# Optimization experiments

Measured on AMD Instinct MI355X. Metric: run time of the kernel, lower is better.

The kernel has to match this reference:

```python
import jax, jax.numpy as jnp
import numpy as np

N = 50000      # nodes
E = 800000     # edges
G = 2000       # graphs
F_IN = 34
HID = 256
H = 8
D = 32         # HID // H
L = 5


def _layer_norm(x, g, b, eps=1e-5):
    m = x.mean(-1, keepdims=True)
    v = ((x - m) ** 2).mean(-1, keepdims=True)
    return (x - m) / jnp.sqrt(v + eps) * g + b


def _gelu(x):
    return jax.nn.gelu(x, approximate=False)  # torch exact GELU


def _segment_softmax(scores, seg, n):
    # scores: [E', H], seg: [E'] target node ids
    m = jax.ops.segment_max(scores, seg, num_segments=n)
    m = jnp.where(jnp.isfinite(m), m, 0.0)
    ex = jnp.exp(scores - m[seg])
    den = jax.ops.segment_sum(ex, seg, num_segments=n)
    return ex / (den[seg] + 1e-16)


def setup_inputs() -> dict:
    key = jax.random.key(0)
    ks = iter(jax.random.split(key, 64))

    def p(shape, fan):
        return (jax.random.normal(next(ks), shape, jnp.float32) / np.sqrt(fan)).astype(jnp.float32)

    inp = {}
    inp['x'] = jax.random.normal(next(ks), (N, F_IN), jnp.float32)
    inp['edge_index'] = jax.random.randint(next(ks), (2, E), 0, N, jnp.int32)
    inp['batch'] = jnp.sort(jax.random.randint(next(ks), (N,), 0, G, jnp.int32))

    # input embed
    inp['in_W'] = p((F_IN, HID), F_IN); inp['in_b'] = jnp.zeros((HID,), jnp.float32)
    inp['in_ln_g'] = jnp.ones((HID,), jnp.float32); inp['in_ln_b'] = jnp.zeros((HID,), jnp.float32)
    # 5 GATv2 layers (stacked on leading dim)
    inp['gat_Wl'] = p((L, HID, HID), HID); inp['gat_bl'] = jnp.zeros((L, HID), jnp.float32)
    inp['gat_Wr'] = p((L, HID, HID), HID); inp['gat_br'] = jnp.zeros((L, HID), jnp.float32)
    inp['gat_att'] = p((L, H, D), D)
    inp['gat_bias'] = jnp.zeros((L, HID), jnp.float32)
    inp['gat_ln_g'] = jnp.ones((L, HID), jnp.float32); inp['gat_ln_b'] = jnp.zeros((L, HID), jnp.float32)
    # TransformerConv
    inp['tr_Wq'] = p((HID, HID), HID); inp['tr_bq'] = jnp.zeros((HID,), jnp.float32)
    inp['tr_Wk'] = p((HID, HID), HID); inp['tr_bk'] = jnp.zeros((HID,), jnp.float32)
    inp['tr_Wv'] = p((HID, HID), HID); inp['tr_bv'] = jnp.zeros((HID,), jnp.float32)
    inp['tr_Wskip'] = p((HID, HID), HID); inp['tr_bskip'] = jnp.zeros((HID,), jnp.float32)
    inp['tr_ln_g'] = jnp.ones((HID,), jnp.float32); inp['tr_ln_b'] = jnp.zeros((HID,), jnp.float32)
    # output proj
    inp['out_W'] = p((2 * HID, 2 * HID), 2 * HID); inp['out_b'] = jnp.zeros((2 * HID,), jnp.float32)
    inp['out_ln_g'] = jnp.ones((2 * HID,), jnp.float32); inp['out_ln_b'] = jnp.zeros((2 * HID,), jnp.float32)
    return inp


def reference(x, edge_index, batch,
              in_W, in_b, in_ln_g, in_ln_b,
              gat_Wl, gat_bl, gat_Wr, gat_br, gat_att, gat_bias, gat_ln_g, gat_ln_b,
              tr_Wq, tr_bq, tr_Wk, tr_bk, tr_Wv, tr_bv, tr_Wskip, tr_bskip, tr_ln_g, tr_ln_b,
              out_W, out_b, out_ln_g, out_ln_b):
    # input embedding (dropout inactive in eval)
    h = _gelu(_layer_norm(x @ in_W + in_b, in_ln_g, in_ln_b))

    src, dst = edge_index[0], edge_index[1]  # PyG: row=source j, col=target i
    loops = jnp.arange(N, dtype=src.dtype)
    s2 = jnp.concatenate([src, loops])  # GATv2 adds self loops
    d2 = jnp.concatenate([dst, loops])

    for l in range(L):  # small fixed loop over layers
        xl = (h @ gat_Wl[l] + gat_bl[l]).reshape(N, H, D)  # source transform / message
        xr = (h @ gat_Wr[l] + gat_br[l]).reshape(N, H, D)  # target transform
        e = jax.nn.leaky_relu(xl[s2] + xr[d2], 0.2)        # [E', H, D]
        score = jnp.einsum('ehd,hd->eh', e, gat_att[l])
        alpha = _segment_softmax(score, d2, N)             # softmax over incoming edges
        out = jax.ops.segment_sum(xl[s2] * alpha[..., None], d2, num_segments=N)
        out = out.reshape(N, HID) + gat_bias[l]
        h = h + _gelu(_layer_norm(out, gat_ln_g[l], gat_ln_b[l]))

    # TransformerConv (no self loops, root_weight skip connection)
    q = (h @ tr_Wq + tr_bq).reshape(N, H, D)
    k = (h @ tr_Wk + tr_bk).reshape(N, H, D)
    v = (h @ tr_Wv + tr_bv).reshape(N, H, D)
    score = (q[dst] * k[src]).sum(-1) / jnp.sqrt(jnp.float32(D))  # [E, H]
    alpha = _segment_softmax(score, dst, N)
    out = jax.ops.segment_sum(v[src] * alpha[..., None], dst, num_segments=N).reshape(N, HID)
    out = out + h @ tr_Wskip + tr_bskip
    h = h + _layer_norm(out, tr_ln_g, tr_ln_b)

    # global mean + max pool
    cnt = jax.ops.segment_sum(jnp.ones((N,), h.dtype), batch, num_segments=G)
    h_mean = jax.ops.segment_sum(h, batch, num_segments=G) / jnp.maximum(cnt, 1.0)[:, None]
    h_max = jax.ops.segment_max(h, batch, num_segments=G)
    h_max = jnp.where(jnp.isfinite(h_max), h_max, 0.0)
    ge = jnp.concatenate([h_mean, h_max], axis=-1)  # [G, 512]
    return _gelu(_layer_norm(ge @ out_W + out_b, out_ln_g, out_ln_b))
```

## Files before the change

kernel.cpp:

```cpp
#include <hip/hip_runtime.h>
#include <math.h>

#define N_NODES 50000
#define N_EDGES 800000
#define N_GRAPH 2000
#define F_INPUT 34
#define HID 256
#define NLAYER 5

typedef __attribute__((ext_vector_type(8))) short short8;
typedef __attribute__((ext_vector_type(4))) float float4v;

__device__ __forceinline__ float gelu_f(float x) {
  return 0.5f * x * (1.0f + erff(x * 0.70710678118654752440f));
}
__device__ __forceinline__ unsigned short bfr(float f) {
  unsigned u = __float_as_uint(f);
  return (unsigned short)((u + 0x7fffu + ((u >> 16) & 1u)) >> 16);
}
__device__ __forceinline__ float b2f(unsigned short s) {
  return __uint_as_float(((unsigned)s) << 16);
}
__device__ __forceinline__ float b2f_lo(unsigned u) {
  return __uint_as_float(u << 16);
}
__device__ __forceinline__ float b2f_hi(unsigned u) {
  return __uint_as_float(u & 0xffff0000u);
}
__device__ __forceinline__ float4 ld4bf(const unsigned short* p) {
  ushort4 u = *(const ushort4*)p;
  float4 f;
  f.x = b2f(u.x); f.y = b2f(u.y); f.z = b2f(u.z); f.w = b2f(u.w);
  return f;
}
__device__ __forceinline__ void acp16(const unsigned short* g, unsigned short* l) {
  __builtin_amdgcn_global_load_lds(
      (const __attribute__((address_space(1))) void*)g,
      (__attribute__((address_space(3))) void*)l, 16, 0, 0);
}

__global__ __launch_bounds__(256) void embed_fused(
    const float* __restrict__ x, const float* __restrict__ W,
    const float* __restrict__ bias, const float* __restrict__ gam,
    const float* __restrict__ bet, float* __restrict__ h,
    unsigned short* __restrict__ hb) {
  __shared__ float xs[16][34];
  __shared__ float ys[16][264];
  int tid = threadIdx.x;
  int r0 = blockIdx.x * 16;
  float* xsf = &xs[0][0];
  for (int i = tid; i < 544; i += 256) xsf[i] = x[(size_t)r0 * 34 + i];
  __syncthreads();
  {
    int rr = tid >> 4;
    int c0 = (tid & 15) * 16;
    float acc[16];
#pragma unroll
    for (int j = 0; j < 16; j += 4) {
      float4 b4 = *(const float4*)&bias[c0 + j];
      acc[j] = b4.x; acc[j + 1] = b4.y; acc[j + 2] = b4.z; acc[j + 3] = b4.w;
    }
    for (int k = 0; k < 34; ++k) {
      float xv = xs[rr][k];
#pragma unroll
      for (int j = 0; j < 16; j += 4) {
        float4 w4 = *(const float4*)&W[(size_t)k * 256 + c0 + j];
        acc[j]     = fmaf(xv, w4.x, acc[j]);
        acc[j + 1] = fmaf(xv, w4.y, acc[j + 1]);
        acc[j + 2] = fmaf(xv, w4.z, acc[j + 2]);
        acc[j + 3] = fmaf(xv, w4.w, acc[j + 3]);
      }
    }
#pragma unroll
    for (int j = 0; j < 16; j += 4) {
      float4 o = {acc[j], acc[j + 1], acc[j + 2], acc[j + 3]};
      *(float4*)&ys[rr][c0 + j] = o;
    }
  }
  __syncthreads();
  int wv = tid >> 6, lane = tid & 63;
  for (int rr = wv * 4; rr < wv * 4 + 4; ++rr) {
    float4 v = *(const float4*)&ys[rr][lane * 4];
    float s = v.x + v.y + v.z + v.w;
    for (int o = 1; o < 64; o <<= 1) s += __shfl_xor(s, o);
    float mean = s * (1.f / 256.f);
    float d0 = v.x - mean, d1 = v.y - mean, d2 = v.z - mean, d3 = v.w - mean;
    float vs = d0 * d0 + d1 * d1 + d2 * d2 + d3 * d3;
    for (int o = 1; o < 64; o <<= 1) vs += __shfl_xor(vs, o);
    float inv = rsqrtf(vs * (1.f / 256.f) + 1e-5f);
    float4 g4 = *(const float4*)&gam[lane * 4];
    float4 b4 = *(const float4*)&bet[lane * 4];
    float y0 = gelu_f(d0 * inv * g4.x + b4.x);
    float y1 = gelu_f(d1 * inv * g4.y + b4.y);
    float y2 = gelu_f(d2 * inv * g4.z + b4.z);
    float y3 = gelu_f(d3 * inv * g4.w + b4.w);
    size_t idx = (size_t)(r0 + rr) * HID + lane * 4;
    float4 o4 = {y0, y1, y2, y3};
    *(float4*)&h[idx] = o4;
    ushort4 ob = {bfr(y0), bfr(y1), bfr(y2), bfr(y3)};
    *(ushort4*)&hb[idx] = ob;
  }
}

__global__ __launch_bounds__(256) void gemm_mfma(
    const unsigned short* __restrict__ A, const unsigned short* __restrict__ Bt,
    const float* __restrict__ bias, void* __restrict__ Cv,
    int M, int Nn, int K, int flags) {
  __shared__ unsigned short smem[16384];
  unsigned short* As = smem;
  unsigned short* Bs = smem + 8192;
  int tid = threadIdx.x;
  int wave = tid >> 6, lane = tid & 63;

  int gx = gridDim.x;
  int flat = blockIdx.y * gx + blockIdx.x;
  int nwg = gx * gridDim.y;
  int xcd = flat & 7, idx = flat >> 3;
  int qb = nwg >> 3, r = nwg & 7;
  int g0 = xcd * qb + min(xcd, r);
  int wk = g0 + idx;
  int row0 = (wk / gx) * 128;
  int col0 = (wk % gx) * 128;

  int wm0 = (wave >> 1) * 64;
  int wn0 = (wave & 1) * 64;
  int q = lane >> 4;
  int ln = lane & 15;

  int srow = wave * 8 + (lane >> 3);
  int scol = ((lane & 7) ^ (lane >> 3)) * 8;
  const unsigned short* pa[4];
  const unsigned short* pb[4];
  unsigned short* la[4];
  unsigned short* lb[4];
#pragma unroll
  for (int i = 0; i < 4; ++i) {
    int ra = min(row0 + srow + i * 32, M - 1);
    pa[i] = A + (size_t)ra * K + scol;
    pb[i] = Bt + (size_t)(col0 + srow + i * 32) * K + scol;
    la[i] = As + (i * 32 + wave * 8) * 64;
    lb[i] = Bs + (i * 32 + wave * 8) * 64;
  }

  float4v acc[4][4];
#pragma unroll
  for (int i = 0; i < 4; ++i)
#pragma unroll
    for (int j = 0; j < 4; ++j) acc[i][j] = (float4v)0.f;

  for (int k0 = 0; k0 < K; k0 += 64) {
#pragma unroll
    for (int i = 0; i < 4; ++i) acp16(pa[i] + k0, la[i]);
#pragma unroll
    for (int i = 0; i < 4; ++i) acp16(pb[i] + k0, lb[i]);
    __syncthreads();
#pragma unroll
    for (int ks = 0; ks < 2; ++ks) {
      int ch = ((ks * 4 + q) ^ (ln & 7)) * 8;
      short8 af[4], bf[4];
#pragma unroll
      for (int i = 0; i < 4; ++i)
        af[i] = *(const short8*)&As[(wm0 + i * 16 + ln) * 64 + ch];
#pragma unroll
      for (int j = 0; j < 4; ++j)
        bf[j] = *(const short8*)&Bs[(wn0 + j * 16 + ln) * 64 + ch];
#pragma unroll
      for (int i = 0; i < 4; ++i)
#pragma unroll
        for (int j = 0; j < 4; ++j)
          acc[i][j] = __builtin_amdgcn_mfma_f32_16x16x32_bf16(af[i], bf[j], acc[i][j], 0, 0, 0);
    }
    __syncthreads();
  }
  int rb = (lane >> 4) * 4;
  if (flags & 2) {
    unsigned short* Cb = (unsigned short*)Cv;
    unsigned short* eb = smem + wave * 2560;
#pragma unroll
    for (int p = 0; p < 2; ++p) {
#pragma unroll
      for (int jj = 0; jj < 2; ++jj) {
        int j = p * 2 + jj;
        float bv = bias[col0 + wn0 + j * 16 + ln];
#pragma unroll
        for (int i = 0; i < 4; ++i)
#pragma unroll
          for (int r2 = 0; r2 < 4; ++r2)
            eb[(i * 16 + rb + r2) * 40 + jj * 16 + ln] = bfr(acc[i][j][r2] + bv);
      }
      int grow = row0 + wm0 + lane;
      uint4 w0 = *(uint4*)&eb[lane * 40 + 0];
      uint4 w1 = *(uint4*)&eb[lane * 40 + 8];
      uint4 w2 = *(uint4*)&eb[lane * 40 + 16];
      uint4 w3 = *(uint4*)&eb[lane * 40 + 24];
      if (grow < M) {
        unsigned short* dst = Cb + (size_t)grow * Nn + col0 + wn0 + p * 32;
        *(uint4*)&dst[0] = w0;
        *(uint4*)&dst[8] = w1;
        *(uint4*)&dst[16] = w2;
        *(uint4*)&dst[24] = w3;
      }
    }
  } else {
    float* C = (float*)Cv;
#pragma unroll
    for (int j = 0; j < 4; ++j) {
      int col = col0 + wn0 + j * 16 + ln;
      float bv = bias[col];
#pragma unroll
      for (int i = 0; i < 4; ++i)
#pragma unroll
        for (int r2 = 0; r2 < 4; ++r2) {
          int row = row0 + wm0 + i * 16 + rb + r2;
          if (row < M) C[(size_t)row * Nn + col] = acc[i][j][r2] + bv;
        }
    }
  }
}

__global__ __launch_bounds__(256) void prep_all(
    const float* __restrict__ Wl, const float* __restrict__ Wr,
    const float* __restrict__ Wq, const float* __restrict__ Wk,
    const float* __restrict__ Wv, const float* __restrict__ Wsk,
    unsigned short* __restrict__ outw,
    const float* __restrict__ Wout, unsigned short* __restrict__ outwout,
    const float* __restrict__ bl, const float* __restrict__ br,
    const float* __restrict__ bq, const float* __restrict__ bk,
    const float* __restrict__ bv, const float* __restrict__ bsk,
    float* __restrict__ bcat) {
  __shared__ float t[32][33];
  int z = blockIdx.z;
  int rr0 = threadIdx.x >> 5, c = threadIdx.x & 31;
  if (z < 14) {
    if (blockIdx.x >= 8 || blockIdx.y >= 8) return;
    const float* W = (z < 10) ? (((z & 1) ? Wr : Wl) + (size_t)(z >> 1) * 65536)
                   : (z == 10) ? Wq : (z == 11) ? Wk : (z == 12) ? Wv : Wsk;
    int k0 = blockIdx.y * 32, n0 = blockIdx.x * 32;
    for (int rr = rr0; rr < 32; rr += 8)
      t[rr][c] = W[(size_t)(k0 + rr) * HID + n0 + c];
    __syncthreads();
    for (int rr = rr0; rr < 32; rr += 8) {
      int n = n0 + rr;
      size_t row;
      if (z == 11)      row = 11 * 256 + (size_t)((n >> 2) * 8 + (n & 3));
      else if (z == 12) row = 11 * 256 + (size_t)((n >> 2) * 8 + 4 + (n & 3));
      else              row = (size_t)z * 256 + n;
      outw[row * HID + k0 + c] = bfr(t[c][rr]);
    }
  } else if (z == 14) {
    int k0 = blockIdx.y * 32, n0 = blockIdx.x * 32;
    for (int rr = rr0; rr < 32; rr += 8)
      t[rr][c] = Wout[(size_t)(k0 + rr) * 512 + n0 + c];
    __syncthreads();
    for (int rr = rr0; rr < 32; rr += 8)
      outwout[(size_t)(n0 + rr) * 512 + k0 + c] = bfr(t[c][rr]);
  } else {
    if (blockIdx.y != 0 || blockIdx.x >= 14) return;
    int i = blockIdx.x * 256 + threadIdx.x;
    if (i < 2560) {
      int l = i >> 9, cc = i & 511;
      bcat[i] = (cc < 256) ? bl[l * 256 + cc] : br[l * 256 + (cc - 256)];
    } else if (i < 3584) {
      int j = i - 2560;
      float v;
      if (j < 256) {
        v = bq[j];
      } else if (j < 768) {
        int p = j - 256;
        int hi = p >> 3, lo = p & 7;
        v = (lo < 4) ? bk[hi * 4 + lo] : bv[hi * 4 + (lo - 4)];
      } else {
        v = bsk[j - 768];
      }
      bcat[i] = v;
    }
  }
}

__global__ __launch_bounds__(256) void ln_act(
    const float* __restrict__ in, const float* __restrict__ gam,
    const float* __restrict__ bet, float* __restrict__ out,
    unsigned short* __restrict__ outb,
    int n_rows, int width, int do_gelu) {
  int wid = blockIdx.x * 4 + (threadIdx.x >> 6);
  int lane = threadIdx.x & 63;
  if (wid >= n_rows) return;
  int chunks = width >> 8;
  float4 v[2];
  float s = 0.f;
  for (int c = 0; c < chunks; ++c) {
    int off = c * 256 + lane * 4;
    float4 t = *(const float4*)&in[(size_t)wid * width + off];
    v[c] = t;
    s += t.x + t.y + t.z + t.w;
  }
  for (int o = 1; o < 64; o <<= 1) s += __shfl_xor(s, o);
  float mean = s / (float)width;
  float vs = 0.f;
  for (int c = 0; c < chunks; ++c) {
    float dx = v[c].x - mean, dy = v[c].y - mean, dz = v[c].z - mean, dw = v[c].w - mean;
    vs += dx * dx + dy * dy + dz * dz + dw * dw;
  }
  for (int o = 1; o < 64; o <<= 1) vs += __shfl_xor(vs, o);
  float inv = rsqrtf(vs / (float)width + 1e-5f);
  for (int c = 0; c < chunks; ++c) {
    int off = c * 256 + lane * 4;
    float4 g4 = *(const float4*)&gam[off];
    float4 b4 = *(const float4*)&bet[off];
    float y[4] = {(v[c].x - mean) * inv * g4.x + b4.x,
                  (v[c].y - mean) * inv * g4.y + b4.y,
                  (v[c].z - mean) * inv * g4.z + b4.z,
                  (v[c].w - mean) * inv * g4.w + b4.w};
    if (do_gelu) {
#pragma unroll
      for (int i = 0; i < 4; ++i) y[i] = gelu_f(y[i]);
    }
    size_t idx = (size_t)wid * width + off;
    float4 o4 = {y[0], y[1], y[2], y[3]};
    *(float4*)&out[idx] = o4;
    if (outb) {
      ushort4 ob = {bfr(y[0]), bfr(y[1]), bfr(y[2]), bfr(y[3])};
      *(ushort4*)&outb[idx] = ob;
    }
  }
}

__global__ __launch_bounds__(256) void edge_count(const int* __restrict__ ei,
                                                  int* __restrict__ counts) {
  int e = blockIdx.x * 256 + threadIdx.x;
  if (e < N_EDGES) atomicAdd(&counts[ei[N_EDGES + e]], 1);
}

__global__ __launch_bounds__(1024) void scan1(const int* __restrict__ counts,
                                              int* __restrict__ indptr,
                                              int* __restrict__ bsums, int n) {
  __shared__ int sm[1024];
  int tid = threadIdx.x;
  int i = blockIdx.x * 1024 + tid;
  int v = (i < n) ? counts[i] : 0;
  sm[tid] = v;
  __syncthreads();
  for (int off = 1; off < 1024; off <<= 1) {
    int t = (tid >= off) ? sm[tid - off] : 0;
    __syncthreads();
    sm[tid] += t;
    __syncthreads();
  }
  if (i < n) indptr[i] = sm[tid] - v;
  if (tid == 1023) bsums[blockIdx.x] = sm[1023];
}

__global__ __launch_bounds__(256) void scan3(const int* __restrict__ bsums,
                                             int* __restrict__ indptr,
                                             int* __restrict__ cursor, int n) {
  __shared__ int pre;
  int i = blockIdx.x * 256 + threadIdx.x;
  if (threadIdx.x == 0) {
    int nb = blockIdx.x >> 2;
    int a = 0;
    for (int j = 0; j < nb; ++j) a += bsums[j];
    pre = a;
  }
  __syncthreads();
  if (i < n) {
    int v = indptr[i] + pre;
    indptr[i] = v;
    cursor[i] = v;
  }
  if (i == 0) indptr[n] = N_EDGES;
}

__global__ __launch_bounds__(256) void edge_scatter(const int* __restrict__ ei,
                                                    int* __restrict__ cursor,
                                                    int* __restrict__ esrc) {
  int e = blockIdx.x * 256 + threadIdx.x;
  if (e < N_EDGES) {
    int d = ei[N_EDGES + e];
    int p = atomicAdd(&cursor[d], 1);
    esrc[p] = ei[e];
  }
}

#define GAT_EDGE(f)                                                        \
  {                                                                        \
    float ex = f.x + xri.x; ex = fmaxf(ex, 0.2f * ex);                     \
    float ey = f.y + xri.y; ey = fmaxf(ey, 0.2f * ey);                     \
    float ez = f.z + xri.z; ez = fmaxf(ez, 0.2f * ez);                     \
    float ew = f.w + xri.w; ew = fmaxf(ew, 0.2f * ew);                     \
    float p = ex * a4.x + ey * a4.y + ez * a4.z + ew * a4.w;               \
    p += __shfl_xor(p, 1); p += __shfl_xor(p, 2); p += __shfl_xor(p, 4);   \
    float wgt = __expf(fminf(p - m0, 60.f));                               \
    ax = fmaf(wgt, f.x, ax); ay = fmaf(wgt, f.y, ay);                      \
    az = fmaf(wgt, f.z, az); aw = fmaf(wgt, f.w, aw);                      \
    lsum += wgt;                                                           \
  }

__global__ __launch_bounds__(256) void gat_agg(
    const unsigned short* __restrict__ xlr, const float* __restrict__ att,
    const int* __restrict__ indptr, const int* __restrict__ esrc,
    const float* __restrict__ pre_bias, const float* __restrict__ gam,
    const float* __restrict__ bet, float* __restrict__ h,
    unsigned short* __restrict__ hb) {
  int wid = blockIdx.x * 4 + (threadIdx.x >> 6);
  int lane = threadIdx.x & 63;
  if (wid >= N_NODES) return;
  float4 xri = ld4bf(&xlr[(size_t)wid * 512 + 256 + lane * 4]);
  float4 a4 = *(const float4*)&att[lane * 4];
  int beg = indptr[wid], end = indptr[wid + 1];

  float m0, lsum, ax, ay, az, aw;
  {
    float4 f = ld4bf(&xlr[(size_t)wid * 512 + lane * 4]);
    float ex = f.x + xri.x; ex = fmaxf(ex, 0.2f * ex);
    float ey = f.y + xri.y; ey = fmaxf(ey, 0.2f * ey);
    float ez = f.z + xri.z; ez = fmaxf(ez, 0.2f * ez);
    float ew = f.w + xri.w; ew = fmaxf(ew, 0.2f * ew);
    float p = ex * a4.x + ey * a4.y + ez * a4.z + ew * a4.w;
    p += __shfl_xor(p, 1); p += __shfl_xor(p, 2); p += __shfl_xor(p, 4);
    m0 = p; lsum = 1.f;
    ax = f.x; ay = f.y; az = f.z; aw = f.w;
  }
  const unsigned short* xbase = xlr + lane * 4;
  int e = beg;
  for (; e + 3 < end; e += 4) {
    int j0 = esrc[e], j1 = esrc[e + 1], j2 = esrc[e + 2], j3 = esrc[e + 3];
    float4 f0 = ld4bf(xbase + (size_t)j0 * 512);
    float4 f1 = ld4bf(xbase + (size_t)j1 * 512);
    float4 f2 = ld4bf(xbase + (size_t)j2 * 512);
    float4 f3 = ld4bf(xbase + (size_t)j3 * 512);
    GAT_EDGE(f0); GAT_EDGE(f1); GAT_EDGE(f2); GAT_EDGE(f3);
  }
  for (; e < end; ++e) {
    int j = esrc[e];
    float4 f = ld4bf(xbase + (size_t)j * 512);
    GAT_EDGE(f);
  }
  float inv = 1.f / (lsum + 1e-16f);
  float4 pb = *(const float4*)&pre_bias[lane * 4];
  float y0 = ax * inv + pb.x, y1 = ay * inv + pb.y;
  float y2 = az * inv + pb.z, y3 = aw * inv + pb.w;
  float s = y0 + y1 + y2 + y3;
  for (int o = 1; o < 64; o <<= 1) s += __shfl_xor(s, o);
  float mean = s * (1.f / 256.f);
  float d0 = y0 - mean, d1 = y1 - mean, d2 = y2 - mean, d3 = y3 - mean;
  float vs = d0 * d0 + d1 * d1 + d2 * d2 + d3 * d3;
  for (int o = 1; o < 64; o <<= 1) vs += __shfl_xor(vs, o);
  float inv2 = rsqrtf(vs * (1.f / 256.f) + 1e-5f);
  float4 g4 = *(const float4*)&gam[lane * 4];
  float4 b4 = *(const float4*)&bet[lane * 4];
  y0 = gelu_f(d0 * inv2 * g4.x + b4.x);
  y1 = gelu_f(d1 * inv2 * g4.y + b4.y);
  y2 = gelu_f(d2 * inv2 * g4.z + b4.z);
  y3 = gelu_f(d3 * inv2 * g4.w + b4.w);
  size_t idx = (size_t)wid * HID + lane * 4;
  float4 r4 = *(const float4*)&h[idx];
  y0 += r4.x; y1 += r4.y; y2 += r4.z; y3 += r4.w;
  float4 o4 = {y0, y1, y2, y3};
  *(float4*)&h[idx] = o4;
  ushort4 ob = {bfr(y0), bfr(y1), bfr(y2), bfr(y3)};
  *(ushort4*)&hb[idx] = ob;
}

#define TR_EDGE(u_)                                                         \
  {                                                                         \
    float p = qi.x * b2f_lo(u_.x);                                          \
    p = fmaf(qi.y, b2f_hi(u_.x), p);                                        \
    p = fmaf(qi.z, b2f_lo(u_.y), p);                                        \
    p = fmaf(qi.w, b2f_hi(u_.y), p);                                        \
    p += __shfl_xor(p, 1); p += __shfl_xor(p, 2); p += __shfl_xor(p, 4);    \
    float wgt = __expf(fminf(p, 60.f));                                     \
    ax = fmaf(wgt, b2f_lo(u_.z), ax); ay = fmaf(wgt, b2f_hi(u_.z), ay);     \
    az = fmaf(wgt, b2f_lo(u_.w), az); aw = fmaf(wgt, b2f_hi(u_.w), aw);     \
    lsum += wgt;                                                            \
  }

__global__ __launch_bounds__(256) void tr_agg(
    const unsigned short* __restrict__ qkv, const int* __restrict__ indptr,
    const int* __restrict__ esrc,
    const float* __restrict__ gam, const float* __restrict__ bet,
    float* __restrict__ h) {
  int wid = blockIdx.x * 4 + (threadIdx.x >> 6);
  int lane = threadIdx.x & 63;
  if (wid >= N_NODES) return;
  const float scale = 0.17677669529663687f;
  float4 qi = ld4bf(&qkv[(size_t)wid * 1024 + lane * 4]);
  qi.x *= scale; qi.y *= scale; qi.z *= scale; qi.w *= scale;
  const unsigned short* kvbase = qkv + 256 + lane * 8;
  int beg = indptr[wid], end = indptr[wid + 1];
  float lsum = 0.f;
  float ax = 0.f, ay = 0.f, az = 0.f, aw = 0.f;
  int e = beg;
  for (; e + 3 < end; e += 4) {
    int j0 = esrc[e], j1 = esrc[e + 1], j2 = esrc[e + 2], j3 = esrc[e + 3];
    uint4 u0 = *(const uint4*)(kvbase + (size_t)j0 * 1024);
    uint4 u1 = *(const uint4*)(kvbase + (size_t)j1 * 1024);
    uint4 u2 = *(const uint4*)(kvbase + (size_t)j2 * 1024);
    uint4 u3 = *(const uint4*)(kvbase + (size_t)j3 * 1024);
    TR_EDGE(u0); TR_EDGE(u1); TR_EDGE(u2); TR_EDGE(u3);
  }
  for (; e < end; ++e) {
    uint4 u0 = *(const uint4*)(kvbase + (size_t)esrc[e] * 1024);
    TR_EDGE(u0);
  }
  float inv = 1.f / (lsum + 1e-16f);
  size_t idx = (size_t)wid * HID + lane * 4;
  float4 sk = ld4bf(&qkv[(size_t)wid * 1024 + 768 + lane * 4]);
  float y0 = ax * inv + sk.x, y1 = ay * inv + sk.y;
  float y2 = az * inv + sk.z, y3 = aw * inv + sk.w;
  float s = y0 + y1 + y2 + y3;
  for (int o = 1; o < 64; o <<= 1) s += __shfl_xor(s, o);
  float mean = s * (1.f / 256.f);
  float d0 = y0 - mean, d1 = y1 - mean, d2 = y2 - mean, d3 = y3 - mean;
  float vs = d0 * d0 + d1 * d1 + d2 * d2 + d3 * d3;
  for (int o = 1; o < 64; o <<= 1) vs += __shfl_xor(vs, o);
  float inv2 = rsqrtf(vs * (1.f / 256.f) + 1e-5f);
  float4 g4 = *(const float4*)&gam[lane * 4];
  float4 b4 = *(const float4*)&bet[lane * 4];
  float4 r4 = *(const float4*)&h[idx];
  float4 o4;
  o4.x = r4.x + d0 * inv2 * g4.x + b4.x;
  o4.y = r4.y + d1 * inv2 * g4.y + b4.y;
  o4.z = r4.z + d2 * inv2 * g4.z + b4.z;
  o4.w = r4.w + d3 * inv2 * g4.w + b4.w;
  *(float4*)&h[idx] = o4;
}

__global__ __launch_bounds__(256) void graph_bounds(const int* __restrict__ batch,
                                                    int* __restrict__ gptr) {
  int i = blockIdx.x * 256 + threadIdx.x;
  if (i >= N_NODES) return;
  int b0 = batch[i];
  if (i == 0)
    for (int g = 0; g <= b0; ++g) gptr[g] = 0;
  int b1 = (i + 1 < N_NODES) ? batch[i + 1] : N_GRAPH;
  for (int g = b0 + 1; g <= b1; ++g) gptr[g] = i + 1;
}

__global__ __launch_bounds__(256) void pool_seg(
    const float* __restrict__ h, const int* __restrict__ gptr,
    unsigned short* __restrict__ geb) {
  int g = blockIdx.x, c = threadIdx.x;
  int s = gptr[g], e = gptr[g + 1];
  float sum = 0.f, mx = -INFINITY;
  for (int r = s; r < e; ++r) {
    float vv = h[(size_t)r * HID + c];
    sum += vv;
    mx = fmaxf(mx, vv);
  }
  int cnt = e - s;
  geb[(size_t)g * 512 + c] = bfr(sum / (float)max(cnt, 1));
  geb[(size_t)g * 512 + 256 + c] = bfr(cnt ? mx : 0.f);
}

static inline void mfma_launch(const unsigned short* A, const unsigned short* Bt,
                               const float* bias, void* C, int M, int Nn, int K,
                               int flags, hipStream_t s) {
  dim3 grid(Nn / 128, (M + 127) / 128);
  gemm_mfma<<<grid, 256, 0, s>>>(A, Bt, bias, C, M, Nn, K, flags);
}

extern "C" void kernel_launch(void* const* d_in, const int* in_sizes, int n_in,
                              void* d_out, int out_size, void* d_ws, size_t ws_size,
                              hipStream_t stream) {
  const float* x       = (const float*)d_in[0];
  const int*   ei      = (const int*)d_in[1];
  const int*   batch   = (const int*)d_in[2];
  const float* in_W    = (const float*)d_in[3];
  const float* in_b    = (const float*)d_in[4];
  const float* in_ln_g = (const float*)d_in[5];
  const float* in_ln_b = (const float*)d_in[6];
  const float* gat_Wl  = (const float*)d_in[7];
  const float* gat_bl  = (const float*)d_in[8];
  const float* gat_Wr  = (const float*)d_in[9];
  const float* gat_br  = (const float*)d_in[10];
  const float* gat_att = (const float*)d_in[11];
  const float* gat_bias= (const float*)d_in[12];
  const float* gat_ln_g= (const float*)d_in[13];
  const float* gat_ln_b= (const float*)d_in[14];
  const float* tr_Wq   = (const float*)d_in[15];
  const float* tr_bq   = (const float*)d_in[16];
  const float* tr_Wk   = (const float*)d_in[17];
  const float* tr_bk   = (const float*)d_in[18];
  const float* tr_Wv   = (const float*)d_in[19];
  const float* tr_bv   = (const float*)d_in[20];
  const float* tr_Wsk  = (const float*)d_in[21];
  const float* tr_bsk  = (const float*)d_in[22];
  const float* tr_ln_g = (const float*)d_in[23];
  const float* tr_ln_b = (const float*)d_in[24];
  const float* out_W   = (const float*)d_in[25];
  const float* out_b   = (const float*)d_in[26];
  const float* out_ln_g= (const float*)d_in[27];
  const float* out_ln_b= (const float*)d_in[28];

  char* w = (char*)d_ws;
  auto take = [&](size_t bytes) -> char* {
    char* p = w;
    w += (bytes + 255) & ~(size_t)255;
    return p;
  };
  const size_t NB = (size_t)N_NODES * HID * sizeof(float);
  float* h    = (float*)take(NB);
  unsigned short* hb  = (unsigned short*)take((size_t)N_NODES * HID * 2);
  unsigned short* xq  = (unsigned short*)take((size_t)N_NODES * 1024 * 2);
  unsigned short* wbuf= (unsigned short*)take((size_t)(14 * 65536 + 262144) * 2);
  float* bcat = (float*)take(3584 * sizeof(float));
  int* indptr = (int*)take((N_NODES + 1) * sizeof(int));
  int* cursor = (int*)take(N_NODES * sizeof(int));
  int* counts = (int*)take(N_NODES * sizeof(int));
  int* esrc   = (int*)take(N_EDGES * sizeof(int));
  int* bsums  = (int*)take(64 * sizeof(int));
  char* w2 = (char*)xq;
  auto take2 = [&](size_t bytes) -> char* {
    char* p = w2;
    w2 += (bytes + 255) & ~(size_t)255;
    return p;
  };
  int* gptr = (int*)take2((N_GRAPH + 1) * sizeof(int));
  unsigned short* geb = (unsigned short*)take2((size_t)N_GRAPH * 512 * 2);
  float* tbuf = (float*)take2((size_t)N_GRAPH * 512 * sizeof(float));

  const int EB = (N_EDGES + 255) / 256;
  const int WB = (N_NODES + 3) / 4;
  const int NSB = (N_NODES + 1023) / 1024;

  {
    dim3 g(16, 16, 16);
    prep_all<<<g, 256, 0, stream>>>(gat_Wl, gat_Wr, tr_Wq, tr_Wk, tr_Wv, tr_Wsk,
                                    wbuf, out_W, wbuf + (size_t)14 * 65536,
                                    gat_bl, gat_br, tr_bq, tr_bk, tr_bv, tr_bsk,
                                    bcat);
  }

  hipMemsetAsync(counts, 0, N_NODES * sizeof(int), stream);
  edge_count<<<EB, 256, 0, stream>>>(ei, counts);
  scan1<<<NSB, 1024, 0, stream>>>(counts, indptr, bsums, N_NODES);
  scan3<<<(N_NODES + 255) / 256, 256, 0, stream>>>(bsums, indptr, cursor, N_NODES);
  edge_scatter<<<EB, 256, 0, stream>>>(ei, cursor, esrc);

  embed_fused<<<N_NODES / 16, 256, 0, stream>>>(x, in_W, in_b, in_ln_g, in_ln_b,
                                                h, hb);

  for (int l = 0; l < NLAYER; ++l) {
    mfma_launch(hb, wbuf + (size_t)(2 * l) * 65536, bcat + l * 512, xq,
                N_NODES, 512, HID, 2, stream);
    gat_agg<<<WB, 256, 0, stream>>>(xq, gat_att + l * HID, indptr, esrc,
                                    gat_bias + l * HID, gat_ln_g + l * HID,
                                    gat_ln_b + l * HID, h, hb);
  }

  mfma_launch(hb, wbuf + (size_t)10 * 65536, bcat + 2560, xq,
              N_NODES, 1024, HID, 2, stream);
  tr_agg<<<WB, 256, 0, stream>>>(xq, indptr, esrc, tr_ln_g, tr_ln_b, h);

  graph_bounds<<<(N_NODES + 255) / 256, 256, 0, stream>>>(batch, gptr);
  pool_seg<<<N_GRAPH, 256, 0, stream>>>(h, gptr, geb);

  mfma_launch(geb, wbuf + (size_t)14 * 65536, out_b, tbuf,
              N_GRAPH, 512, 512, 0, stream);
  ln_act<<<(N_GRAPH + 3) / 4, 256, 0, stream>>>(tbuf, out_ln_g, out_ln_b,
                                                (float*)d_out, nullptr,
                                                N_GRAPH, 512, 1);
}
```

Baseline: 1.140 ms.

## Store GAT projections head-major and aggregate per head with split LayerNorm

The GEMM gains a flag that writes its bf16 output in head-major blocks of 32 columns, so each head's xl/xr rows are contiguous. GAT aggregation becomes one block per (node-group, head), with 8 lane groups each taking every eighth edge, a software-prefetched gather of 64-byte rows, and a cross-group reduction. The aim is gathers that touch only one head's working set, which should improve cache locality, at the cost of 8x more blocks. LayerNorm, GELU and the residual move into a separate kernel that goes through an extra fp32 buffer round trip. The graph_bounds kernel is dropped in favour of a per-block binary search over the sorted batch array.

```diff
diff --git a/kernel.cpp b/kernel.cpp
--- a/kernel.cpp
+++ b/kernel.cpp
@@ -194,7 +194,12 @@
       uint4 w2 = *(uint4*)&eb[lane * 40 + 16];
       uint4 w3 = *(uint4*)&eb[lane * 40 + 24];
       if (grow < M) {
-        unsigned short* dst = Cb + (size_t)grow * Nn + col0 + wn0 + p * 32;
+        int cb = col0 + wn0 + p * 32;
+        unsigned short* dst;
+        if (flags & 4)
+          dst = Cb + ((size_t)(cb >> 5) * M + grow) * 32;
+        else
+          dst = Cb + (size_t)grow * Nn + cb;
         *(uint4*)&dst[0] = w0;
         *(uint4*)&dst[8] = w1;
         *(uint4*)&dst[16] = w2;
@@ -381,7 +386,7 @@
   }
 }
 
-#define GAT_EDGE(f)                                                        \
+#define GAT_EDGE2(f)                                                       \
   {                                                                        \
     float ex = f.x + xri.x; ex = fmaxf(ex, 0.2f * ex);                     \
     float ey = f.y + xri.y; ey = fmaxf(ey, 0.2f * ey);                     \
@@ -395,63 +400,85 @@
     lsum += wgt;                                                           \
   }
 
-__global__ __launch_bounds__(256) void gat_agg(
-    const unsigned short* __restrict__ xlr, const float* __restrict__ att,
+__global__ __launch_bounds__(256) void gat_agg2(
+    const unsigned short* __restrict__ xq, const float* __restrict__ att,
     const int* __restrict__ indptr, const int* __restrict__ esrc,
-    const float* __restrict__ pre_bias, const float* __restrict__ gam,
+    const float* __restrict__ pre_bias, float* __restrict__ hpre) {
+  int b = blockIdx.x;
+  int h = b & 7;
+  int wid = (b >> 3) * 4 + (threadIdx.x >> 6);
+  if (wid >= N_NODES) return;
+  int lane = threadIdx.x & 63;
+  int g = lane >> 3;
+  int d4 = (lane & 7) * 4;
+
+  const unsigned short* xlp = xq + (size_t)h * N_NODES * 32;
+  const unsigned short* xrp = xq + (size_t)(8 + h) * N_NODES * 32;
+  float4 xri = ld4bf(xrp + (size_t)wid * 32 + d4);
+  float4 a4 = *(const float4*)&att[h * 32 + d4];
+
+  float4 fs = ld4bf(xlp + (size_t)wid * 32 + d4);
+  float m0;
+  {
+    float ex = fs.x + xri.x; ex = fmaxf(ex, 0.2f * ex);
+    float ey = fs.y + xri.y; ey = fmaxf(ey, 0.2f * ey);
+    float ez = fs.z + xri.z; ez = fmaxf(ez, 0.2f * ez);
+    float ew = fs.w + xri.w; ew = fmaxf(ew, 0.2f * ew);
+    float p = ex * a4.x + ey * a4.y + ez * a4.z + ew * a4.w;
+    p += __shfl_xor(p, 1); p += __shfl_xor(p, 2); p += __shfl_xor(p, 4);
+    m0 = p;
+  }
+
+  int beg = indptr[wid], end = indptr[wid + 1];
+  float lsum = 0.f, ax = 0.f, ay = 0.f, az = 0.f, aw = 0.f;
+  int e0 = beg + g;
+  float4 fcur;
+  bool vcur = (e0 < end);
+  if (vcur) fcur = ld4bf(xlp + (size_t)esrc[e0] * 32 + d4);
+  while (vcur) {
+    int e1 = e0 + 8;
+    float4 fnxt;
+    bool vnxt = (e1 < end);
+    if (vnxt) fnxt = ld4bf(xlp + (size_t)esrc[e1] * 32 + d4);
+    GAT_EDGE2(fcur);
+    e0 = e1; fcur = fnxt; vcur = vnxt;
+  }
+  for (int o = 8; o < 64; o <<= 1) {
+    ax += __shfl_xor(ax, o); ay += __shfl_xor(ay, o);
+    az += __shfl_xor(az, o); aw += __shfl_xor(aw, o);
+    lsum += __shfl_xor(lsum, o);
+  }
+  ax += fs.x; ay += fs.y; az += fs.z; aw += fs.w;
+  lsum += 1.f;
+  float inv = 1.f / (lsum + 1e-16f);
+  float4 pb = *(const float4*)&pre_bias[h * 32 + d4];
+  if (g == 0) {
+    float4 o4 = {ax * inv + pb.x, ay * inv + pb.y, az * inv + pb.z, aw * inv + pb.w};
+    *(float4*)&hpre[(size_t)wid * 256 + h * 32 + d4] = o4;
+  }
+}
+
+__global__ __launch_bounds__(256) void ln_resid(
+    const float* __restrict__ hpre, const float* __restrict__ gam,
     const float* __restrict__ bet, float* __restrict__ h,
     unsigned short* __restrict__ hb) {
   int wid = blockIdx.x * 4 + (threadIdx.x >> 6);
   int lane = threadIdx.x & 63;
   if (wid >= N_NODES) return;
-  float4 xri = ld4bf(&xlr[(size_t)wid * 512 + 256 + lane * 4]);
-  float4 a4 = *(const float4*)&att[lane * 4];
-  int beg = indptr[wid], end = indptr[wid + 1];
-
-  float m0, lsum, ax, ay, az, aw;
-  {
-    float4 f = ld4bf(&xlr[(size_t)wid * 512 + lane * 4]);
-    float ex = f.x + xri.x; ex = fmaxf(ex, 0.2f * ex);
-    float ey = f.y + xri.y; ey = fmaxf(ey, 0.2f * ey);
-    float ez = f.z + xri.z; ez = fmaxf(ez, 0.2f * ez);
-    float ew = f.w + xri.w; ew = fmaxf(ew, 0.2f * ew);
-    float p = ex * a4.x + ey * a4.y + ez * a4.z + ew * a4.w;
-    p += __shfl_xor(p, 1); p += __shfl_xor(p, 2); p += __shfl_xor(p, 4);
-    m0 = p; lsum = 1.f;
-    ax = f.x; ay = f.y; az = f.z; aw = f.w;
-  }
-  const unsigned short* xbase = xlr + lane * 4;
-  int e = beg;
-  for (; e + 3 < end; e += 4) {
-    int j0 = esrc[e], j1 = esrc[e + 1], j2 = esrc[e + 2], j3 = esrc[e + 3];
-    float4 f0 = ld4bf(xbase + (size_t)j0 * 512);
-    float4 f1 = ld4bf(xbase + (size_t)j1 * 512);
-    float4 f2 = ld4bf(xbase + (size_t)j2 * 512);
-    float4 f3 = ld4bf(xbase + (size_t)j3 * 512);
-    GAT_EDGE(f0); GAT_EDGE(f1); GAT_EDGE(f2); GAT_EDGE(f3);
-  }
-  for (; e < end; ++e) {
-    int j = esrc[e];
-    float4 f = ld4bf(xbase + (size_t)j * 512);
-    GAT_EDGE(f);
-  }
-  float inv = 1.f / (lsum + 1e-16f);
-  float4 pb = *(const float4*)&pre_bias[lane * 4];
-  float y0 = ax * inv + pb.x, y1 = ay * inv + pb.y;
-  float y2 = az * inv + pb.z, y3 = aw * inv + pb.w;
-  float s = y0 + y1 + y2 + y3;
+  float4 v = *(const float4*)&hpre[(size_t)wid * 256 + lane * 4];
+  float s = v.x + v.y + v.z + v.w;
   for (int o = 1; o < 64; o <<= 1) s += __shfl_xor(s, o);
   float mean = s * (1.f / 256.f);
-  float d0 = y0 - mean, d1 = y1 - mean, d2 = y2 - mean, d3 = y3 - mean;
+  float d0 = v.x - mean, d1 = v.y - mean, d2 = v.z - mean, d3 = v.w - mean;
   float vs = d0 * d0 + d1 * d1 + d2 * d2 + d3 * d3;
   for (int o = 1; o < 64; o <<= 1) vs += __shfl_xor(vs, o);
   float inv2 = rsqrtf(vs * (1.f / 256.f) + 1e-5f);
   float4 g4 = *(const float4*)&gam[lane * 4];
   float4 b4 = *(const float4*)&bet[lane * 4];
-  y0 = gelu_f(d0 * inv2 * g4.x + b4.x);
-  y1 = gelu_f(d1 * inv2 * g4.y + b4.y);
-  y2 = gelu_f(d2 * inv2 * g4.z + b4.z);
-  y3 = gelu_f(d3 * inv2 * g4.w + b4.w);
+  float y0 = gelu_f(d0 * inv2 * g4.x + b4.x);
+  float y1 = gelu_f(d1 * inv2 * g4.y + b4.y);
+  float y2 = gelu_f(d2 * inv2 * g4.z + b4.z);
+  float y3 = gelu_f(d3 * inv2 * g4.w + b4.w);
   size_t idx = (size_t)wid * HID + lane * 4;
   float4 r4 = *(const float4*)&h[idx];
   y0 += r4.x; y1 += r4.y; y2 += r4.z; y3 += r4.w;
@@ -525,22 +552,16 @@
   *(float4*)&h[idx] = o4;
 }
 
-__global__ __launch_bounds__(256) void graph_bounds(const int* __restrict__ batch,
-                                                    int* __restrict__ gptr) {
-  int i = blockIdx.x * 256 + threadIdx.x;
-  if (i >= N_NODES) return;
-  int b0 = batch[i];
-  if (i == 0)
-    for (int g = 0; g <= b0; ++g) gptr[g] = 0;
-  int b1 = (i + 1 < N_NODES) ? batch[i + 1] : N_GRAPH;
-  for (int g = b0 + 1; g <= b1; ++g) gptr[g] = i + 1;
-}
-
 __global__ __launch_bounds__(256) void pool_seg(
-    const float* __restrict__ h, const int* __restrict__ gptr,
+    const float* __restrict__ h, const int* __restrict__ batch,
     unsigned short* __restrict__ geb) {
   int g = blockIdx.x, c = threadIdx.x;
-  int s = gptr[g], e = gptr[g + 1];
+  int lo = 0, hi = N_NODES;
+  while (lo < hi) { int m = (lo + hi) >> 1; if (batch[m] < g) lo = m + 1; else hi = m; }
+  int s = lo;
+  hi = N_NODES;
+  while (lo < hi) { int m = (lo + hi) >> 1; if (batch[m] < g + 1) lo = m + 1; else hi = m; }
+  int e = lo;
   float sum = 0.f, mx = -INFINITY;
   for (int r = s; r < e; ++r) {
     float vv = h[(size_t)r * HID + c];
@@ -600,6 +621,7 @@
   };
   const size_t NB = (size_t)N_NODES * HID * sizeof(float);
   float* h    = (float*)take(NB);
+  float* hpre = (float*)take(NB);
   unsigned short* hb  = (unsigned short*)take((size_t)N_NODES * HID * 2);
   unsigned short* xq  = (unsigned short*)take((size_t)N_NODES * 1024 * 2);
   unsigned short* wbuf= (unsigned short*)take((size_t)(14 * 65536 + 262144) * 2);
@@ -615,7 +637,6 @@
     w2 += (bytes + 255) & ~(size_t)255;
     return p;
   };
-  int* gptr = (int*)take2((N_GRAPH + 1) * sizeof(int));
   unsigned short* geb = (unsigned short*)take2((size_t)N_GRAPH * 512 * 2);
   float* tbuf = (float*)take2((size_t)N_GRAPH * 512 * sizeof(float));
 
@@ -642,18 +663,19 @@
 
   for (int l = 0; l < NLAYER; ++l) {
     mfma_launch(hb, wbuf + (size_t)(2 * l) * 65536, bcat + l * 512, xq,
-                N_NODES, 512, HID, 2, stream);
-    gat_agg<<<WB, 256, 0, stream>>>(xq, gat_att + l * HID, indptr, esrc,
-                                    gat_bias + l * HID, gat_ln_g + l * HID,
-                                    gat_ln_b + l * HID, h, hb);
+                N_NODES, 512, HID, 2 | 4, stream);
+    gat_agg2<<<8 * (N_NODES / 4), 256, 0, stream>>>(xq, gat_att + l * HID,
+                                                    indptr, esrc,
+                                                    gat_bias + l * HID, hpre);
+    ln_resid<<<WB, 256, 0, stream>>>(hpre, gat_ln_g + l * HID, gat_ln_b + l * HID,
+                                     h, hb);
   }
 
   mfma_launch(hb, wbuf + (size_t)10 * 65536, bcat + 2560, xq,
               N_NODES, 1024, HID, 2, stream);
   tr_agg<<<WB, 256, 0, stream>>>(xq, indptr, esrc, tr_ln_g, tr_ln_b, h);
 
-  graph_bounds<<<(N_NODES + 255) / 256, 256, 0, stream>>>(batch, gptr);
-  pool_seg<<<N_GRAPH, 256, 0, stream>>>(h, gptr, geb);
+  pool_seg<<<N_GRAPH, 256, 0, stream>>>(h, batch, geb);
 
   mfma_launch(geb, wbuf + (size_t)14 * 65536, out_b, tbuf,
               N_GRAPH, 512, 512, 0, stream);
```

Measured after the change: 1.753 ms. 1.54x slower.
